# Kernel tuning notes

Measured on AMD Instinct MI355X. Metric: run time of the kernel, lower is better.

Reference implementation:

```python
import jax, jax.numpy as jnp
import numpy as np

B, N, DIM = 1, 4096, 1024
HEADS, DIM_HEAD = 12, 8
POST_LOG_SCALE = 1.0
SCALE = DIM_HEAD ** -0.5


def setup_inputs() -> dict:
    key = jax.random.key(0)
    kx, kw = jax.random.split(key)
    x = jax.random.normal(kx, (B, N, DIM), dtype=jnp.float32)
    # torch nn.Linear(dim, heads*dim_head*2, bias=False) weight: [2*heads*dim_head, dim]
    W = jax.random.normal(kw, (2 * HEADS * DIM_HEAD, DIM), dtype=jnp.float32) * (DIM ** -0.5)
    return {"x": x, "W": W}


def reference(x, W):
    b, n, _ = x.shape
    # linear: x @ W^T -> [b, n, 2*h*d]; rearrange '(qk h d) -> qk b h n d'
    proj = jnp.einsum('bnc,oc->bno', x, W)
    proj = proj.reshape(b, n, 2, HEADS, DIM_HEAD)
    q = jnp.transpose(proj[:, :, 0], (0, 2, 1, 3))  # [b, h, n, d]
    k = jnp.transpose(proj[:, :, 1], (0, 2, 1, 3))  # [b, h, n, d]
    # small-d QK matmul -> [b, h, n, n]
    gates = jnp.einsum('bhid,bhjd->bhij', q, k) * SCALE
    gates = jax.nn.log_sigmoid(gates) * POST_LOG_SCALE
    # causal_mask = triu(ones, diagonal=0); masked_fill -> zero on/above diagonal
    i = jnp.arange(n)[:, None]
    j = jnp.arange(n)[None, :]
    keep = j < i  # strictly lower-triangular entries survive
    gates = jnp.where(keep, gates, 0.0)
    # flip-cumsum-flip == reverse cumulative sum along last axis
    gates = jax.lax.cumsum(gates, axis=3, reverse=True)
    return gates
```

## Files before the change

kernel.cpp:

```cpp
#include <hip/hip_runtime.h>

#define NTOK 4096
#define DIMC 1024
#define HEADS 12
#define DH 8
#define QSCALE 0.35355339059327373f
#define LOG2E  1.4426950408889634f
#define LN2    0.6931471805599453f

typedef float f4 __attribute__((ext_vector_type(4)));

#define KOFF (HEADS * NTOK * DH)

__global__ __launch_bounds__(256) void k1_proj(const float* __restrict__ x,
                                               const float* __restrict__ W,
                                               float* __restrict__ qk) {
    __shared__ float xs[8 * 1028];
    const int t = threadIdx.x;
    const int row0 = blockIdx.x * 8;

    const f4* x4 = (const f4*)(x + (size_t)row0 * DIMC);
    #pragma unroll
    for (int i = 0; i < 8; ++i) {
        int f = t + i * 256;
        int r = f >> 8;
        int c4 = f & 255;
        f4 v = x4[f];
        *(f4*)(&xs[r * 1028 + c4 * 4]) = v;
    }
    __syncthreads();

    const int g  = t >> 2;
    const int rg = t & 3;

    float acc[2][3];
    #pragma unroll
    for (int a = 0; a < 2; ++a)
        #pragma unroll
        for (int m = 0; m < 3; ++m) acc[a][m] = 0.f;

    const float* w0 = W + (size_t)(3 * g) * DIMC;
    #pragma unroll 2
    for (int c = 0; c < DIMC; c += 4) {
        f4 w[3];
        #pragma unroll
        for (int m = 0; m < 3; ++m)
            w[m] = *(const f4*)(w0 + (size_t)m * DIMC + c);
        #pragma unroll
        for (int a = 0; a < 2; ++a) {
            f4 xv = *(const f4*)(&xs[(rg * 2 + a) * 1028 + c]);
            #pragma unroll
            for (int m = 0; m < 3; ++m) {
                acc[a][m] = fmaf(xv.x, w[m].x,
                            fmaf(xv.y, w[m].y,
                            fmaf(xv.z, w[m].z,
                            fmaf(xv.w, w[m].w, acc[a][m]))));
            }
        }
    }

    #pragma unroll
    for (int m = 0; m < 3; ++m) {
        int o   = 3 * g + m;
        int qkf = (o >= 96) ? 1 : 0;
        int oo  = o - 96 * qkf;
        int h   = oo >> 3;
        int d   = oo & 7;
        #pragma unroll
        for (int a = 0; a < 2; ++a) {
            int n = row0 + rg * 2 + a;
            float v = acc[a][m];
            if (!qkf) {
                qk[((size_t)h * NTOK + n) * DH + d] = v * QSCALE;
            } else {
                qk[KOFF + ((size_t)h * DH + d) * NTOK + n] = v;
            }
        }
    }
}

__device__ __forceinline__ float log_sigmoid(float s) {
    float mn = fminf(s, 0.f);
    float z  = __builtin_amdgcn_exp2f(fabsf(s) * -LOG2E);
    return mn - LN2 * __builtin_amdgcn_logf(1.f + z);
}

__global__ __launch_bounds__(256) void k2_gates(const float* __restrict__ qk,
                                                float* __restrict__ out) {
    const int bid  = blockIdx.x;
    const int h    = bid >> 8;
    const int i0   = (bid & 255) << 4;
    const int t    = threadIdx.x;
    const int lane = t & 63;
    const int wid  = t >> 6;
    const int r0   = i0 + 4 * wid;

    float qr[4][8];
    #pragma unroll
    for (int r = 0; r < 4; ++r) {
        const float* qp = qk + ((size_t)h * NTOK + r0 + r) * DH;
        #pragma unroll
        for (int d = 0; d < 8; ++d) qr[r][d] = qp[d];
    }

    const float* ks = qk + KOFF + (size_t)h * DH * NTOK;
    float* ob = out + ((size_t)h * NTOK + r0) * NTOK;

    const int ccmax = (r0 + 3) >> 8;

    f4 z = (f4)(0.f);
    for (int cc = 15; cc > ccmax; --cc) {
        const int j0 = cc * 256 + 4 * lane;
        #pragma unroll
        for (int r = 0; r < 4; ++r)
            __builtin_nontemporal_store(z, (f4*)(ob + (size_t)r * NTOK + j0));
    }

    float carry[4];
    #pragma unroll
    for (int r = 0; r < 4; ++r) carry[r] = 0.f;

    for (int cc = ccmax; cc >= 0; --cc) {
        const int j0 = cc * 256 + 4 * lane;

        f4 kv[8];
        #pragma unroll
        for (int d = 0; d < 8; ++d)
            kv[d] = *(const f4*)(ks + (size_t)d * NTOK + j0);

        float g[4][4], tot[4], s[4];
        #pragma unroll
        for (int r = 0; r < 4; ++r) {
            float a0 = 0.f, a1 = 0.f, a2 = 0.f, a3 = 0.f;
            #pragma unroll
            for (int d = 0; d < 8; ++d) {
                const float qd = qr[r][d];
                a0 = fmaf(qd, kv[d].x, a0);
                a1 = fmaf(qd, kv[d].y, a1);
                a2 = fmaf(qd, kv[d].z, a2);
                a3 = fmaf(qd, kv[d].w, a3);
            }
            const int ir = r0 + r;
            float g0 = (j0 + 0 < ir) ? log_sigmoid(a0) : 0.f;
            float g1 = (j0 + 1 < ir) ? log_sigmoid(a1) : 0.f;
            float g2 = (j0 + 2 < ir) ? log_sigmoid(a2) : 0.f;
            float g3 = (j0 + 3 < ir) ? log_sigmoid(a3) : 0.f;
            g2 += g3; g1 += g2; g0 += g1;
            g[r][0] = g0; g[r][1] = g1; g[r][2] = g2; g[r][3] = g3;
            tot[r] = g0; s[r] = g0;
        }

        #pragma unroll
        for (int off = 1; off < 64; off <<= 1) {
            float v0 = __shfl_down(s[0], off, 64);
            float v1 = __shfl_down(s[1], off, 64);
            float v2 = __shfl_down(s[2], off, 64);
            float v3 = __shfl_down(s[3], off, 64);
            if (lane + off < 64) { s[0] += v0; s[1] += v1; s[2] += v2; s[3] += v3; }
        }

        #pragma unroll
        for (int r = 0; r < 4; ++r) {
            const float base = (s[r] - tot[r]) + carry[r];
            carry[r] += __builtin_amdgcn_readfirstlane(s[r]);
            f4 v;
            v.x = g[r][0] + base;
            v.y = g[r][1] + base;
            v.z = g[r][2] + base;
            v.w = g[r][3] + base;
            __builtin_nontemporal_store(v, (f4*)(ob + (size_t)r * NTOK + j0));
        }
    }
}

extern "C" void kernel_launch(void* const* d_in, const int* in_sizes, int n_in,
                              void* d_out, int out_size, void* d_ws, size_t ws_size,
                              hipStream_t stream) {
    const float* x = (const float*)d_in[0];
    const float* W = (const float*)d_in[1];
    float* out = (float*)d_out;
    float* qk  = (float*)d_ws;

    hipLaunchKernelGGL(k1_proj, dim3(NTOK / 8), dim3(256), 0, stream, x, W, qk);
    hipLaunchKernelGGL(k2_gates, dim3(HEADS * NTOK / 16), dim3(256), 0, stream, qk, out);
}
```

Baseline: 216.1 us.

## Restructure gates kernel to one row per wave with LDS double-buffered K tiles

The gates kernel now assigns one output row per wavefront and four rows per block, four times as many blocks as before. Each block stages 256-column K tiles, stored in a new tiled layout, through a double-buffered LDS buffer with a prefetch and a barrier per step. The log2e factor is folded into Q in the projection, the ln2 factor is applied once at the store, and the causal mask is only evaluated on the diagonal tile. Packed two-wide FMAs are used in both kernels. The changes aim to cut per-element transcendental and mask overhead and improve occupancy, at the cost of block-wide syncs per tile and fewer rows sharing each K load.

```diff
diff --git a/kernel.cpp b/kernel.cpp
--- a/kernel.cpp
+++ b/kernel.cpp
@@ -7,8 +7,10 @@
 #define QSCALE 0.35355339059327373f
 #define LOG2E  1.4426950408889634f
 #define LN2    0.6931471805599453f
+#define QPRE   (QSCALE * LOG2E)
 
 typedef float f4 __attribute__((ext_vector_type(4)));
+typedef float f2 __attribute__((ext_vector_type(2)));
 
 #define KOFF (HEADS * NTOK * DH)
 
@@ -33,11 +35,11 @@
     const int g  = t >> 2;
     const int rg = t & 3;
 
-    float acc[2][3];
+    f2 acc[2][3];
     #pragma unroll
     for (int a = 0; a < 2; ++a)
         #pragma unroll
-        for (int m = 0; m < 3; ++m) acc[a][m] = 0.f;
+        for (int m = 0; m < 3; ++m) acc[a][m] = (f2)(0.f);
 
     const float* w0 = W + (size_t)(3 * g) * DIMC;
     #pragma unroll 2
@@ -51,10 +53,8 @@
             f4 xv = *(const f4*)(&xs[(rg * 2 + a) * 1028 + c]);
             #pragma unroll
             for (int m = 0; m < 3; ++m) {
-                acc[a][m] = fmaf(xv.x, w[m].x,
-                            fmaf(xv.y, w[m].y,
-                            fmaf(xv.z, w[m].z,
-                            fmaf(xv.w, w[m].w, acc[a][m]))));
+                acc[a][m] = __builtin_elementwise_fma(xv.xy, w[m].xy, acc[a][m]);
+                acc[a][m] = __builtin_elementwise_fma(xv.zw, w[m].zw, acc[a][m]);
             }
         }
     }
@@ -69,107 +69,106 @@
         #pragma unroll
         for (int a = 0; a < 2; ++a) {
             int n = row0 + rg * 2 + a;
-            float v = acc[a][m];
+            float v = acc[a][m].x + acc[a][m].y;
             if (!qkf) {
-                qk[((size_t)h * NTOK + n) * DH + d] = v * QSCALE;
+                qk[((size_t)h * NTOK + n) * DH + d] = v * QPRE;
             } else {
-                qk[KOFF + ((size_t)h * DH + d) * NTOK + n] = v;
+                qk[KOFF + (((size_t)h * 16 + (n >> 8)) * DH + d) * 256 + (n & 255)] = v;
             }
         }
     }
 }
 
-__device__ __forceinline__ float log_sigmoid(float s) {
-    float mn = fminf(s, 0.f);
-    float z  = __builtin_amdgcn_exp2f(fabsf(s) * -LOG2E);
-    return mn - LN2 * __builtin_amdgcn_logf(1.f + z);
+__device__ __forceinline__ float lsig2(float u) {
+    float mn = fminf(u, 0.f);
+    float z  = __builtin_amdgcn_exp2f(-fabsf(u));
+    return mn - __builtin_amdgcn_logf(1.f + z);
 }
 
 __global__ __launch_bounds__(256) void k2_gates(const float* __restrict__ qk,
                                                 float* __restrict__ out) {
     const int bid  = blockIdx.x;
-    const int h    = bid >> 8;
-    const int i0   = (bid & 255) << 4;
+    const int h    = bid >> 10;
+    const int r0   = (bid & 1023) << 2;
     const int t    = threadIdx.x;
     const int lane = t & 63;
-    const int wid  = t >> 6;
-    const int r0   = i0 + 4 * wid;
+    const int w    = t >> 6;
+    const int r    = r0 + w;
 
-    float qr[4][8];
+    __shared__ float ks[2][8 * 256];
+
+    const float* qp = qk + ((size_t)h * NTOK + r) * DH;
+    float qs[8];
     #pragma unroll
-    for (int r = 0; r < 4; ++r) {
-        const float* qp = qk + ((size_t)h * NTOK + r0 + r) * DH;
-        #pragma unroll
-        for (int d = 0; d < 8; ++d) qr[r][d] = qp[d];
-    }
+    for (int d = 0; d < 8; ++d) qs[d] = qp[d];
 
-    const float* ks = qk + KOFF + (size_t)h * DH * NTOK;
-    float* ob = out + ((size_t)h * NTOK + r0) * NTOK;
-
-    const int ccmax = (r0 + 3) >> 8;
+    float* o = out + ((size_t)h * NTOK + r) * NTOK;
+    const int cb = r0 >> 8;
+    const int rm = r & 255;
 
     f4 z = (f4)(0.f);
-    for (int cc = 15; cc > ccmax; --cc) {
-        const int j0 = cc * 256 + 4 * lane;
-        #pragma unroll
-        for (int r = 0; r < 4; ++r)
-            __builtin_nontemporal_store(z, (f4*)(ob + (size_t)r * NTOK + j0));
+    for (int cc = 15; cc > cb; --cc)
+        __builtin_nontemporal_store(z, (f4*)(o + cc * 256 + 4 * lane));
+
+    {
+        const float* kt = qk + KOFF + ((size_t)h * 16 + cb) * 2048;
+        f4 a = *(const f4*)(kt + 4 * t);
+        f4 b = *(const f4*)(kt + 4 * t + 1024);
+        *(f4*)(&ks[0][4 * t]) = a;
+        *(f4*)(&ks[0][4 * t + 1024]) = b;
     }
+    __syncthreads();
 
-    float carry[4];
-    #pragma unroll
-    for (int r = 0; r < 4; ++r) carry[r] = 0.f;
+    float carry = 0.f;
+    int p = 0;
 
-    for (int cc = ccmax; cc >= 0; --cc) {
-        const int j0 = cc * 256 + 4 * lane;
+    for (int c = cb; c >= 0; --c) {
+        const int cn = (c > 0) ? (c - 1) : 0;
+        const float* kt = qk + KOFF + ((size_t)h * 16 + cn) * 2048;
+        f4 sa = *(const f4*)(kt + 4 * t);
+        f4 sb = *(const f4*)(kt + 4 * t + 1024);
 
         f4 kv[8];
         #pragma unroll
         for (int d = 0; d < 8; ++d)
-            kv[d] = *(const f4*)(ks + (size_t)d * NTOK + j0);
+            kv[d] = *(const f4*)(&ks[p][d * 256 + 4 * lane]);
 
-        float g[4][4], tot[4], s[4];
+        f2 A = (f2)(0.f), B = (f2)(0.f);
         #pragma unroll
-        for (int r = 0; r < 4; ++r) {
-            float a0 = 0.f, a1 = 0.f, a2 = 0.f, a3 = 0.f;
-            #pragma unroll
-            for (int d = 0; d < 8; ++d) {
-                const float qd = qr[r][d];
-                a0 = fmaf(qd, kv[d].x, a0);
-                a1 = fmaf(qd, kv[d].y, a1);
-                a2 = fmaf(qd, kv[d].z, a2);
-                a3 = fmaf(qd, kv[d].w, a3);
-            }
-            const int ir = r0 + r;
-            float g0 = (j0 + 0 < ir) ? log_sigmoid(a0) : 0.f;
-            float g1 = (j0 + 1 < ir) ? log_sigmoid(a1) : 0.f;
-            float g2 = (j0 + 2 < ir) ? log_sigmoid(a2) : 0.f;
-            float g3 = (j0 + 3 < ir) ? log_sigmoid(a3) : 0.f;
-            g2 += g3; g1 += g2; g0 += g1;
-            g[r][0] = g0; g[r][1] = g1; g[r][2] = g2; g[r][3] = g3;
-            tot[r] = g0; s[r] = g0;
+        for (int d = 0; d < 8; ++d) {
+            A = __builtin_elementwise_fma(kv[d].xy, (f2)(qs[d]), A);
+            B = __builtin_elementwise_fma(kv[d].zw, (f2)(qs[d]), B);
         }
 
+        float g[4];
+        if (c == cb) {
+            g[0] = (4 * lane + 0 < rm) ? lsig2(A.x) : 0.f;
+            g[1] = (4 * lane + 1 < rm) ? lsig2(A.y) : 0.f;
+            g[2] = (4 * lane + 2 < rm) ? lsig2(B.x) : 0.f;
+            g[3] = (4 * lane + 3 < rm) ? lsig2(B.y) : 0.f;
+        } else {
+            g[0] = lsig2(A.x); g[1] = lsig2(A.y);
+            g[2] = lsig2(B.x); g[3] = lsig2(B.y);
+        }
+
+        g[2] += g[3]; g[1] += g[2]; g[0] += g[1];
+        const float tot = g[0];
+        float s = tot;
         #pragma unroll
         for (int off = 1; off < 64; off <<= 1) {
-            float v0 = __shfl_down(s[0], off, 64);
-            float v1 = __shfl_down(s[1], off, 64);
-            float v2 = __shfl_down(s[2], off, 64);
-            float v3 = __shfl_down(s[3], off, 64);
-            if (lane + off < 64) { s[0] += v0; s[1] += v1; s[2] += v2; s[3] += v3; }
+            float v = __shfl_down(s, off, 64);
+            if (lane + off < 64) s += v;
         }
+        const float base = (s - tot) + carry;
+        carry += __builtin_amdgcn_readfirstlane(s);
 
-        #pragma unroll
-        for (int r = 0; r < 4; ++r) {
-            const float base = (s[r] - tot[r]) + carry[r];
-            carry[r] += __builtin_amdgcn_readfirstlane(s[r]);
-            f4 v;
-            v.x = g[r][0] + base;
-            v.y = g[r][1] + base;
-            v.z = g[r][2] + base;
-            v.w = g[r][3] + base;
-            __builtin_nontemporal_store(v, (f4*)(ob + (size_t)r * NTOK + j0));
-        }
+        f4 gv = {g[0], g[1], g[2], g[3]};
+        __builtin_nontemporal_store((gv + base) * LN2, (f4*)(o + c * 256 + 4 * lane));
+
+        *(f4*)(&ks[p ^ 1][4 * t]) = sa;
+        *(f4*)(&ks[p ^ 1][4 * t + 1024]) = sb;
+        __syncthreads();
+        p ^= 1;
     }
 }
 
@@ -182,5 +181,5 @@
     float* qk  = (float*)d_ws;
 
     hipLaunchKernelGGL(k1_proj, dim3(NTOK / 8), dim3(256), 0, stream, x, W, qk);
-    hipLaunchKernelGGL(k2_gates, dim3(HEADS * NTOK / 16), dim3(256), 0, stream, qk, out);
+    hipLaunchKernelGGL(k2_gates, dim3(HEADS * NTOK / 4), dim3(256), 0, stream, qk, out);
 }
```

Measured after the change: 201.2 us. 6.9% less time.
